# Optimization experiments

Measured on AMD Instinct MI355X. Metric: run time of the kernel, lower is better.

Reference implementation:

```python
import jax, jax.numpy as jnp
import numpy as np

N_EMBD = 1024
B, T = 4, 2048

def setup_inputs() -> dict:
    key = jax.random.key(0)
    k1, k2, k3, k4 = jax.random.split(key, 4)
    s = 1.0 / np.sqrt(N_EMBD)
    return {
        "x": jax.random.normal(k1, (B, T, N_EMBD), dtype=jnp.float32),
        "Wq": jax.random.normal(k2, (N_EMBD, N_EMBD), dtype=jnp.float32) * s,
        "Wk": jax.random.normal(k3, (N_EMBD, N_EMBD), dtype=jnp.float32) * s,
        "Wv": jax.random.normal(k4, (N_EMBD, N_EMBD), dtype=jnp.float32) * s,
    }

def reference(x, Wq, Wk, Wv):
    # x: [B,T,C]; torch Linear (no bias): y = x @ W.T
    Bq, Tq, C = x.shape
    q = jnp.einsum('btc,dc->btd', x, Wq)
    k = jnp.einsum('btc,dc->btd', x, Wk)
    v = jnp.einsum('btc,dc->btd', x, Wv)
    att = jnp.einsum('bqd,bkd->bqk', q, k) / jnp.sqrt(jnp.float32(C))
    causal = jnp.tril(jnp.ones((Tq, Tq), dtype=bool))  # [T,T]
    att = jnp.where(causal, att, -jnp.inf)
    w = jax.nn.softmax(att, axis=-1)
    # dropout is identity in eval mode
    out = jnp.einsum('bqk,bkd->bqd', w, v)
    return out
```

## Files before the change

### kernel.cpp

```cpp
#include <hip/hip_runtime.h>
#include <stdint.h>

typedef __attribute__((ext_vector_type(8))) __bf16 bf16x8;
typedef __attribute__((ext_vector_type(8))) unsigned short ushort8;
typedef __attribute__((ext_vector_type(4))) float f32x4;

static __device__ __forceinline__ unsigned short f2bf(float f) {
  unsigned u = __float_as_uint(f);
  u += 0x7fffu + ((u >> 16) & 1u);
  return (unsigned short)(u >> 16);
}

union U16cast { ushort8 u; bf16x8 b; };
static __device__ __forceinline__ bf16x8 as_bf16x8(ushort8 x) { U16cast t; t.u = x; return t.b; }
static __device__ __forceinline__ bf16x8 ldfrag(const unsigned short* p) {
  return as_bf16x8(*(const ushort8*)p);
}

#define GLD_LDS16(g, l)                                                        \
  __builtin_amdgcn_global_load_lds(                                            \
      (const __attribute__((address_space(1))) void*)(g),                      \
      (__attribute__((address_space(3))) void*)(l), 16, 0, 0)

__global__ __launch_bounds__(256) void cast_all(
    const float* __restrict__ x, const float* __restrict__ Wq,
    const float* __restrict__ Wk, const float* __restrict__ Wv,
    unsigned short* __restrict__ out, float* __restrict__ lzero,
    long nx4, long nw4, long n4) {
  long g = (long)blockIdx.x * blockDim.x + threadIdx.x;
  if (g < 2048) ((float4*)lzero)[g] = (float4){0.f, 0.f, 0.f, 0.f};
  long i = g;
  long stride = (long)gridDim.x * blockDim.x;
  for (; i < n4; i += stride) {
    const float4* src;
    long j = i;
    if (j < nx4) {
      src = (const float4*)x;
    } else {
      j -= nx4;
      if (j < nw4) src = (const float4*)Wq;
      else if (j < 2 * nw4) { src = (const float4*)Wk; j -= nw4; }
      else { src = (const float4*)Wv; j -= 2 * nw4; }
    }
    float4 v = src[j];
    ushort4 o;
    o.x = f2bf(v.x); o.y = f2bf(v.y); o.z = f2bf(v.z); o.w = f2bf(v.w);
    *(ushort4*)(out + i * 4) = o;
  }
}

__global__ __launch_bounds__(512, 4) void gemm_qkv(
    const unsigned short* __restrict__ A, const unsigned short* __restrict__ B,
    unsigned short* __restrict__ qkv, unsigned short* __restrict__ vT) {
  __shared__ __align__(16) unsigned short As[2][4096];
  __shared__ __align__(16) unsigned short Bs[2][8192];

  int wg = blockIdx.x;
  wg = (wg & 7) * 96 + (wg >> 3);
  const int bm = wg / 12, bn = wg % 12;
  const int m0 = bm << 7, n0 = bn << 8;

  const int tid = threadIdx.x;

  const int srow = tid >> 2;
  const int sseg = (tid & 3) ^ ((srow >> 1) & 3);
  const unsigned short* sa = A + (long)(m0 + srow) * 1024 + sseg * 8;
  const unsigned short* sb0 = B + (long)(n0 + srow) * 1024 + sseg * 8;
  const unsigned short* sb1 = sb0 + (long)128 * 1024;
  unsigned short* dA = &As[0][0] + tid * 8;
  unsigned short* dB = &Bs[0][0] + tid * 8;

#define STG(kt, s)                                                             \
  do {                                                                         \
    GLD_LDS16(sa + (kt) * 32, dA + (s) * 4096);                                \
    GLD_LDS16(sb0 + (kt) * 32, dB + (s) * 8192);                               \
    GLD_LDS16(sb1 + (kt) * 32, dB + (s) * 8192 + 4096);                        \
  } while (0)

  const int lane = tid & 63;
  const int w = tid >> 6;
  const int wr = w >> 2;
  const int wc = w & 3;
  const int fr = lane & 15;
  const int kb = lane >> 4;
  const int segr = (kb ^ ((fr >> 1) & 3)) << 3;
  const unsigned short* rA = &As[0][0] + (wr * 64 + fr) * 32 + segr;
  const unsigned short* rB = &Bs[0][0] + (wc * 64 + fr) * 32 + segr;

  f32x4 acc[4][4];
#pragma unroll
  for (int mf = 0; mf < 4; ++mf)
#pragma unroll
    for (int nf = 0; nf < 4; ++nf)
      acc[mf][nf] = (f32x4){0.f, 0.f, 0.f, 0.f};

  STG(0, 0);
  __syncthreads();

  for (int kt = 0; kt < 32; ++kt) {
    const int s = kt & 1;
    if (kt + 1 < 32) STG(kt + 1, s ^ 1);

    const unsigned short* pA = rA + s * 4096;
    const unsigned short* pB = rB + s * 8192;
    bf16x8 av[4], bv[4];
#pragma unroll
    for (int mf = 0; mf < 4; ++mf) av[mf] = ldfrag(pA + mf * 512);
#pragma unroll
    for (int nf = 0; nf < 4; ++nf) bv[nf] = ldfrag(pB + nf * 512);

#pragma unroll
    for (int mf = 0; mf < 4; ++mf)
#pragma unroll
      for (int nf = 0; nf < 4; ++nf)
        acc[mf][nf] = __builtin_amdgcn_mfma_f32_16x16x32_bf16(av[mf], bv[nf], acc[mf][nf], 0, 0, 0);

    __syncthreads();
  }
#undef STG

  const int rq = kb << 2;
  if (n0 < 2048) {
#pragma unroll
    for (int mf = 0; mf < 4; ++mf) {
      const int row = m0 + wr * 64 + mf * 16 + rq;
#pragma unroll
      for (int nf = 0; nf < 4; ++nf) {
        const int col = n0 + wc * 64 + nf * 16 + fr;
#pragma unroll
        for (int r = 0; r < 4; ++r)
          qkv[(long)(row + r) * 3072 + col] = f2bf(acc[mf][nf][r]);
      }
    }
  } else {
    const int b2 = m0 >> 11;
    const int t0 = (m0 & 2047) + wr * 64;
#pragma unroll
    for (int mf = 0; mf < 4; ++mf) {
      const int trow = t0 + mf * 16 + rq;
#pragma unroll
      for (int nf = 0; nf < 4; ++nf) {
        const int colv = (n0 - 2048) + wc * 64 + nf * 16 + fr;
        ushort4 o;
        o.x = f2bf(acc[mf][nf][0]); o.y = f2bf(acc[mf][nf][1]);
        o.z = f2bf(acc[mf][nf][2]); o.w = f2bf(acc[mf][nf][3]);
        *(ushort4*)(vT + ((long)b2 * 1024 + colv) * 2048 + trow) = o;
      }
    }
  }
}

template <int MODE>
__global__ __launch_bounds__(256, 4) void gemm128(
    const unsigned short* __restrict__ A, const unsigned short* __restrict__ Bp,
    void* __restrict__ Cout, float* __restrict__ lbuf) {
  __shared__ __align__(16) unsigned short As[2][4096];
  __shared__ __align__(16) unsigned short Bs[2][4096];

  constexpr int LDA = (MODE == 1) ? 3072 : 2048;

  const int wgid = blockIdx.x;
  int m0, n0, b;
  if constexpr (MODE == 1) {
    b = wgid & 3;
    const int t = wgid >> 2;
    int bm = 0;
    while ((bm + 2) * (bm + 1) / 2 <= t) ++bm;
    const int bn = t - bm * (bm + 1) / 2;
    m0 = bm << 7; n0 = bn << 7;
  } else {
    const int xcd = wgid & 7;
    const int inner = wgid >> 3;
    const int s = inner >> 5;
    const int rem = inner & 31;
    b = rem >> 3;
    const int bn = rem & 7;
    const int bm = s ? (15 - xcd) : xcd;
    m0 = bm << 7; n0 = bn << 7;
  }

  const unsigned short* Ab = A;
  const unsigned short* Bb = Bp;
  if constexpr (MODE == 1) {
    Ab += (long)b * 2048 * 3072;
    Bb += (long)b * 2048 * 3072;
  } else {
    Ab += (long)b * 2048 * 2048;
    Bb += (long)b * 1024 * 2048;
  }

  const int tid = threadIdx.x;

  const int srow = tid >> 2;
  const int sseg = (tid & 3) ^ ((srow >> 1) & 3);
  const unsigned short* sa = Ab + (long)(m0 + srow) * LDA + sseg * 8;
  const unsigned short* sb = Bb + (long)(n0 + srow) * LDA + sseg * 8;
  const long sRj = (long)64 * LDA;
  unsigned short* dA = &As[0][0] + tid * 8;
  unsigned short* dB = &Bs[0][0] + tid * 8;

#define STG(kt, s)                                                             \
  do {                                                                         \
    GLD_LDS16(sa + (kt) * 32, dA + (s) * 4096);                                \
    GLD_LDS16(sa + sRj + (kt) * 32, dA + (s) * 4096 + 2048);                   \
    GLD_LDS16(sb + (kt) * 32, dB + (s) * 4096);                                \
    GLD_LDS16(sb + sRj + (kt) * 32, dB + (s) * 4096 + 2048);                   \
  } while (0)

  const int lane = tid & 63;
  const int w = tid >> 6;
  const int wr = w >> 1;
  const int wc = w & 1;
  const int fr = lane & 15;
  const int kb = lane >> 4;
  const unsigned short* rA0 = &As[0][0] + wr * 64 * 32;
  const unsigned short* rB0 = &Bs[0][0] + wc * 64 * 32;

  f32x4 acc[4][4];
#pragma unroll
  for (int mf = 0; mf < 4; ++mf)
#pragma unroll
    for (int nf = 0; nf < 4; ++nf)
      acc[mf][nf] = (f32x4){0.f, 0.f, 0.f, 0.f};

  const int kend = (MODE == 2) ? (m0 + 128) : 1024;
  const int NT = kend >> 5;

  STG(0, 0);
  __syncthreads();

  for (int kt = 0; kt < NT; ++kt) {
    const int s = kt & 1;
    if (kt + 1 < NT) STG(kt + 1, s ^ 1);

    bf16x8 av[4], bv[4];
#pragma unroll
    for (int mf = 0; mf < 4; ++mf) {
      const int row = mf * 16 + fr;
      const int segr = (kb ^ ((row >> 1) & 3)) << 3;
      av[mf] = ldfrag(rA0 + s * 4096 + row * 32 + segr);
    }
#pragma unroll
    for (int nf = 0; nf < 4; ++nf) {
      const int row = nf * 16 + fr;
      const int segr = (kb ^ ((row >> 1) & 3)) << 3;
      bv[nf] = ldfrag(rB0 + s * 4096 + row * 32 + segr);
    }

#pragma unroll
    for (int mf = 0; mf < 4; ++mf)
#pragma unroll
      for (int nf = 0; nf < 4; ++nf)
        acc[mf][nf] = __builtin_amdgcn_mfma_f32_16x16x32_bf16(av[mf], bv[nf], acc[mf][nf], 0, 0, 0);

    __syncthreads();
  }
#undef STG

  const int rq = kb << 2;
  if constexpr (MODE == 1) {
    unsigned short* Pu = (unsigned short*)Cout + (long)b * 2048 * 2048;
    float* lrow = lbuf + b * 2048;
#pragma unroll
    for (int mf = 0; mf < 4; ++mf) {
      const int row = m0 + wr * 64 + mf * 16 + rq;
      float psum0 = 0.f, psum1 = 0.f, psum2 = 0.f, psum3 = 0.f;
#pragma unroll
      for (int nf = 0; nf < 4; ++nf) {
        const int col = n0 + wc * 64 + nf * 16 + fr;
        float e0 = (col > row + 0) ? 0.f : __expf(acc[mf][nf][0] * 0.03125f);
        float e1 = (col > row + 1) ? 0.f : __expf(acc[mf][nf][1] * 0.03125f);
        float e2 = (col > row + 2) ? 0.f : __expf(acc[mf][nf][2] * 0.03125f);
        float e3 = (col > row + 3) ? 0.f : __expf(acc[mf][nf][3] * 0.03125f);
        psum0 += e0; psum1 += e1; psum2 += e2; psum3 += e3;
        Pu[(long)(row + 0) * 2048 + col] = f2bf(e0);
        Pu[(long)(row + 1) * 2048 + col] = f2bf(e1);
        Pu[(long)(row + 2) * 2048 + col] = f2bf(e2);
        Pu[(long)(row + 3) * 2048 + col] = f2bf(e3);
      }
#pragma unroll
      for (int off = 1; off < 16; off <<= 1) {
        psum0 += __shfl_xor(psum0, off);
        psum1 += __shfl_xor(psum1, off);
        psum2 += __shfl_xor(psum2, off);
        psum3 += __shfl_xor(psum3, off);
      }
      if (fr == 0) {
        atomicAdd(&lrow[row + 0], psum0);
        atomicAdd(&lrow[row + 1], psum1);
        atomicAdd(&lrow[row + 2], psum2);
        atomicAdd(&lrow[row + 3], psum3);
      }
    }
  } else {
    float* Cf = (float*)Cout + (long)b * 2048 * 1024;
    const float* lrow = lbuf + b * 2048;
#pragma unroll
    for (int mf = 0; mf < 4; ++mf) {
      const int row = m0 + wr * 64 + mf * 16 + rq;
      float il0 = 1.0f / lrow[row + 0];
      float il1 = 1.0f / lrow[row + 1];
      float il2 = 1.0f / lrow[row + 2];
      float il3 = 1.0f / lrow[row + 3];
#pragma unroll
      for (int nf = 0; nf < 4; ++nf) {
        const int col = n0 + wc * 64 + nf * 16 + fr;
        Cf[(long)(row + 0) * 1024 + col] = acc[mf][nf][0] * il0;
        Cf[(long)(row + 1) * 1024 + col] = acc[mf][nf][1] * il1;
        Cf[(long)(row + 2) * 1024 + col] = acc[mf][nf][2] * il2;
        Cf[(long)(row + 3) * 1024 + col] = acc[mf][nf][3] * il3;
      }
    }
  }
}

extern "C" void kernel_launch(void* const* d_in, const int* in_sizes, int n_in,
                              void* d_out, int out_size, void* d_ws, size_t ws_size,
                              hipStream_t stream) {
  const float* x  = (const float*)d_in[0];
  const float* Wq = (const float*)d_in[1];
  const float* Wk = (const float*)d_in[2];
  const float* Wv = (const float*)d_in[3];
  float* out = (float*)d_out;

  const int Bb = 4, T = 2048, C = 1024;
  const long BT = (long)Bb * T;
  const int N3 = 3 * C;

  char* ws = (char*)d_ws;
  unsigned short* xb   = (unsigned short*)ws; ws += BT * C * 2;
  unsigned short* wbuf = (unsigned short*)ws; ws += (long)N3 * C * 2;
  unsigned short* qkv  = (unsigned short*)ws; ws += BT * N3 * 2;
  unsigned short* vT   = (unsigned short*)ws; ws += BT * C * 2;
  unsigned short* Pu   = (unsigned short*)ws; ws += (long)Bb * T * T * 2;
  float* lbuf          = (float*)ws;          ws += BT * 4;

  const long nx4 = BT * C / 4, nw4 = (long)C * C / 4;
  cast_all<<<2048, 256, 0, stream>>>(x, Wq, Wk, Wv, xb, lbuf, nx4, nw4, nx4 + 3 * nw4);

  gemm_qkv<<<dim3(768, 1, 1), 512, 0, stream>>>(xb, wbuf, qkv, vT);

  gemm128<1><<<dim3(544, 1, 1), 256, 0, stream>>>(qkv, qkv + C, Pu, lbuf);

  gemm128<2><<<dim3(512, 1, 1), 256, 0, stream>>>(Pu, vT, out, lbuf);
}
```

Before: 155.8 us.

## Triple-buffer QKV GEMM with split-phase loads, explicit waitcnts and setprio

Moves the QKV projection GEMM from double to triple LDS buffering, prefetching two k-tiles ahead. Each iteration is split into two halves that interleave LDS fragment reads, global-to-LDS staging and MFMA clusters, with explicit vmcnt/lgkmcnt waits, raw s_barriers, sched_barriers and s_setprio around the MFMA blocks. The aim is to hide global load latency and keep the matrix cores busy. In exchange LDS use per block grows, which may lower occupancy, and the hand-placed waitcnts risk ordering mistakes.

New measurement: 157.5 us. About the same (+1.1%).

```diff
diff --git a/kernel.cpp b/kernel.cpp
--- a/kernel.cpp
+++ b/kernel.cpp
@@ -52,8 +52,8 @@
 __global__ __launch_bounds__(512, 4) void gemm_qkv(
     const unsigned short* __restrict__ A, const unsigned short* __restrict__ B,
     unsigned short* __restrict__ qkv, unsigned short* __restrict__ vT) {
-  __shared__ __align__(16) unsigned short As[2][4096];
-  __shared__ __align__(16) unsigned short Bs[2][8192];
+  __shared__ __align__(16) unsigned short As[3][4096];
+  __shared__ __align__(16) unsigned short Bs[3][8192];
 
   int wg = blockIdx.x;
   wg = (wg & 7) * 96 + (wg >> 3);
@@ -70,12 +70,9 @@
   unsigned short* dA = &As[0][0] + tid * 8;
   unsigned short* dB = &Bs[0][0] + tid * 8;
 
-#define STG(kt, s)                                                             \
-  do {                                                                         \
-    GLD_LDS16(sa + (kt) * 32, dA + (s) * 4096);                                \
-    GLD_LDS16(sb0 + (kt) * 32, dB + (s) * 8192);                               \
-    GLD_LDS16(sb1 + (kt) * 32, dB + (s) * 8192 + 4096);                        \
-  } while (0)
+#define STG_SA(kt, s)  GLD_LDS16(sa + (kt) * 32, dA + (s) * 4096)
+#define STG_SB0(kt, s) GLD_LDS16(sb0 + (kt) * 32, dB + (s) * 8192)
+#define STG_SB1(kt, s) GLD_LDS16(sb1 + (kt) * 32, dB + (s) * 8192 + 4096)
 
   const int lane = tid & 63;
   const int w = tid >> 6;
@@ -94,30 +91,70 @@
     for (int nf = 0; nf < 4; ++nf)
       acc[mf][nf] = (f32x4){0.f, 0.f, 0.f, 0.f};
 
-  STG(0, 0);
-  __syncthreads();
-
+  STG_SA(0, 0); STG_SB0(0, 0); STG_SB1(0, 0);
+  STG_SA(1, 1); STG_SB0(1, 1); STG_SB1(1, 1);
+  asm volatile("s_waitcnt vmcnt(3)" ::: "memory");
+  __builtin_amdgcn_s_barrier();
+  __builtin_amdgcn_sched_barrier(0);
+
+  int c0 = 0, c2 = 2;
+#pragma unroll 1
   for (int kt = 0; kt < 32; ++kt) {
-    const int s = kt & 1;
-    if (kt + 1 < 32) STG(kt + 1, s ^ 1);
-
-    const unsigned short* pA = rA + s * 4096;
-    const unsigned short* pB = rB + s * 8192;
-    bf16x8 av[4], bv[4];
+    const unsigned short* pA = rA + c0 * 4096;
+    const unsigned short* pB = rB + c0 * 8192;
+    bf16x8 av[4], bv0, bv1, bv2, bv3;
+
 #pragma unroll
     for (int mf = 0; mf < 4; ++mf) av[mf] = ldfrag(pA + mf * 512);
-#pragma unroll
-    for (int nf = 0; nf < 4; ++nf) bv[nf] = ldfrag(pB + nf * 512);
-
-#pragma unroll
-    for (int mf = 0; mf < 4; ++mf)
-#pragma unroll
-      for (int nf = 0; nf < 4; ++nf)
-        acc[mf][nf] = __builtin_amdgcn_mfma_f32_16x16x32_bf16(av[mf], bv[nf], acc[mf][nf], 0, 0, 0);
-
-    __syncthreads();
-  }
-#undef STG
+    bv0 = ldfrag(pB);
+    bv1 = ldfrag(pB + 512);
+    if (kt < 30) {
+      STG_SA(kt + 2, c2);
+      STG_SB0(kt + 2, c2);
+      asm volatile("s_waitcnt vmcnt(3)" ::: "memory");
+    } else {
+      asm volatile("s_waitcnt vmcnt(0)" ::: "memory");
+    }
+    __builtin_amdgcn_s_barrier();
+    asm volatile("s_waitcnt lgkmcnt(0)" ::: "memory");
+    __builtin_amdgcn_sched_barrier(0);
+    __builtin_amdgcn_s_setprio(1);
+#pragma unroll
+    for (int mf = 0; mf < 4; ++mf) {
+      acc[mf][0] = __builtin_amdgcn_mfma_f32_16x16x32_bf16(av[mf], bv0, acc[mf][0], 0, 0, 0);
+      acc[mf][1] = __builtin_amdgcn_mfma_f32_16x16x32_bf16(av[mf], bv1, acc[mf][1], 0, 0, 0);
+    }
+    __builtin_amdgcn_s_setprio(0);
+    __builtin_amdgcn_s_barrier();
+    __builtin_amdgcn_sched_barrier(0);
+
+    bv2 = ldfrag(pB + 1024);
+    bv3 = ldfrag(pB + 1536);
+    if (kt < 30) {
+      STG_SB1(kt + 2, c2);
+      asm volatile("s_waitcnt vmcnt(3)" ::: "memory");
+    } else {
+      asm volatile("s_waitcnt vmcnt(0)" ::: "memory");
+    }
+    __builtin_amdgcn_s_barrier();
+    asm volatile("s_waitcnt lgkmcnt(0)" ::: "memory");
+    __builtin_amdgcn_sched_barrier(0);
+    __builtin_amdgcn_s_setprio(1);
+#pragma unroll
+    for (int mf = 0; mf < 4; ++mf) {
+      acc[mf][2] = __builtin_amdgcn_mfma_f32_16x16x32_bf16(av[mf], bv2, acc[mf][2], 0, 0, 0);
+      acc[mf][3] = __builtin_amdgcn_mfma_f32_16x16x32_bf16(av[mf], bv3, acc[mf][3], 0, 0, 0);
+    }
+    __builtin_amdgcn_s_setprio(0);
+    __builtin_amdgcn_s_barrier();
+    __builtin_amdgcn_sched_barrier(0);
+
+    c0 = (c0 == 2) ? 0 : c0 + 1;
+    c2 = (c2 == 2) ? 0 : c2 + 1;
+  }
+#undef STG_SA
+#undef STG_SB0
+#undef STG_SB1
 
   const int rq = kb << 2;
   if (n0 < 2048) {
@@ -233,7 +270,7 @@
     const int s = kt & 1;
     if (kt + 1 < NT) STG(kt + 1, s ^ 1);
 
-    bf16x8 av[4], bv[4];
+    bf16x8 av[4], bvv[4];
 #pragma unroll
     for (int mf = 0; mf < 4; ++mf) {
       const int row = mf * 16 + fr;
@@ -244,14 +281,14 @@
     for (int nf = 0; nf < 4; ++nf) {
       const int row = nf * 16 + fr;
       const int segr = (kb ^ ((row >> 1) & 3)) << 3;
-      bv[nf] = ldfrag(rB0 + s * 4096 + row * 32 + segr);
+      bvv[nf] = ldfrag(rB0 + s * 4096 + row * 32 + segr);
     }
 
 #pragma unroll
     for (int mf = 0; mf < 4; ++mf)
 #pragma unroll
       for (int nf = 0; nf < 4; ++nf)
-        acc[mf][nf] = __builtin_amdgcn_mfma_f32_16x16x32_bf16(av[mf], bv[nf], acc[mf][nf], 0, 0, 0);
+        acc[mf][nf] = __builtin_amdgcn_mfma_f32_16x16x32_bf16(av[mf], bvv[nf], acc[mf][nf], 0, 0, 0);
 
     __syncthreads();
   }
```
